# Kernel optimization log

Hardware: AMD Instinct MI355X
Metric: run time of the kernel (lower is better)

The kernel has to match this reference:

```python
import jax, jax.numpy as jnp
import numpy as np

B, Q, N, H, W = 8, 4096, 128, 256, 256
ALPHA = 0.4      # adaptive-bandwidth coefficient
EOS = 0.5        # eos_coef -> empty_weight[0]
DIV_THRS = 0.5   # div threshold for dense stride
EPS = 1e-5


def setup_inputs() -> dict:
    key = jax.random.key(0)
    k = jax.random.split(key, 8)
    pred_logits = jax.random.normal(k[0], (B, Q, 2), jnp.float32)
    pred_points = jax.random.uniform(k[1], (B, Q, 2), jnp.float32)  # normalized [0,1)
    # GT points in pixel coords (col0 scaled by H, col1 by W, matching the code's normalization quirk)
    tgt_points = jax.random.uniform(k[2], (B, N, 2), jnp.float32) * jnp.array([H, W], jnp.float32)
    split_map = jax.random.uniform(k[3], (B, Q), jnp.float32)
    den = jax.random.uniform(k[4], (B,), jnp.float32)
    prob = jax.random.uniform(k[5], (B, 1, H, W), jnp.float32)
    prob_est = jax.random.uniform(k[6], (B, 1, H, W), jnp.float32)
    src_idx = jax.random.randint(k[7], (B, N), 0, Q)  # matched query index per GT point
    labels = jnp.ones((B, N), jnp.int32)  # single foreground class = 1
    return dict(pred_logits=pred_logits, pred_points=pred_points, tgt_points=tgt_points,
                split_map=split_map, den=den, prob=prob, prob_est=prob_est,
                src_idx=src_idx, labels=labels)


def _density_map(tp_norm, batch_idx):
    """Adaptive-bandwidth Gaussian splatting (vectorized KDTree + conv2d replacement).
    tp_norm: (M,2) normalized points; batch_idx: (M,) int. Returns (B,H,W)."""
    M = tp_norm.shape[0]
    # integer pixel locations, as in the original (round + clip before KDTree)
    px = jnp.clip(jnp.round(tp_norm[:, 0] * W), 0, W - 1)
    py = jnp.clip(jnp.round(tp_norm[:, 1] * H), 0, H - 1)
    pts = jnp.stack([px, py], axis=1).reshape(B, N, 2)  # (B,N,2) float pixel coords
    # per-batch pairwise distances -> 4-NN (self included)
    d2 = jnp.sum((pts[:, :, None, :] - pts[:, None, :, :]) ** 2, axis=-1)  # (B,N,N)
    dist = jnp.sqrt(jnp.maximum(d2, 0.0))
    neg_d, nn_idx = jax.lax.top_k(-dist, 4)          # ascending distances
    dists = -neg_d                                    # (B,N,4); [...,0] = self = 0
    di = dists[..., 1]                                # nearest-neighbor distance (B,N)
    nbr = nn_idx[..., 1:]                             # (B,N,3) neighbor indices
    nbr_d = jnp.take_along_axis(jnp.broadcast_to(di[:, None, :], (B, N, N)), nbr, axis=2)
    d_mtop3 = jnp.mean(nbr_d, axis=-1)                # mean of neighbors' NN distances
    d = jnp.minimum(di, d_mtop3)
    sigma = jnp.maximum(ALPHA * d, 1.0).reshape(M)    # (M,)
    # truncation window: kernel_size = int(6*sigma), forced odd; half = ks // 2
    ks = (6.0 * sigma).astype(jnp.int32)
    ks = jnp.where(ks % 2 == 0, ks + 1, ks)
    half = (ks // 2).astype(jnp.float32)              # (M,)
    # peak-normalized truncated Gaussian == exp(-r^2/(2 sigma^2)) inside the kernel window
    yy = jnp.arange(H, dtype=jnp.float32)
    xx = jnp.arange(W, dtype=jnp.float32)
    dyv = yy[None, :] - py[:, None]                   # (M,H)
    dxv = xx[None, :] - px[:, None]                   # (M,W)
    r2 = dyv[:, :, None] ** 2 + dxv[:, None, :] ** 2  # (M,H,W)
    inside = (jnp.abs(dyv) <= half[:, None])[:, :, None] & (jnp.abs(dxv) <= half[:, None])[:, None, :]
    maps = jnp.where(inside, jnp.exp(-r2 / (2.0 * (sigma ** 2)[:, None, None])), 0.0)
    # density = elementwise max over points of a batch (zeros where no point contributes)
    dens = jax.ops.segment_max(maps, batch_idx, num_segments=B, indices_are_sorted=True)
    return jnp.maximum(dens, 0.0)                     # (B,H,W)


def reference(pred_logits, pred_points, tgt_points, split_map, den, prob, prob_est, src_idx, labels):
    f32 = jnp.float32
    batch_idx = jnp.repeat(jnp.arange(B), N)          # (M,)
    src_flat = src_idx.reshape(-1)                    # (M,)

    # ---------------- loss_labels (div variant) ----------------
    target_classes = jnp.zeros((B, Q), jnp.int32).at[batch_idx, src_flat].set(labels.reshape(-1))
    logp = jax.nn.log_softmax(pred_logits, axis=-1)
    raw_ce = -jnp.take_along_axis(logp, target_classes[..., None], axis=-1)[..., 0]  # (B,Q)
    weights = jnp.where(target_classes == 0, EOS, 1.0).astype(f32)
    order = jnp.argsort(den)
    is_sp = jnp.zeros((B,), bool).at[order[B // 2:]].set(True)  # sparse = denser-half images
    sp = is_sp.astype(f32)[:, None]
    ds = 1.0 - sp
    div_m = (split_map > DIV_THRS).astype(f32)
    ndiv_m = (split_map <= DIV_THRS).astype(f32)
    wdm = weights * div_m
    loss_ce = ((raw_ce * wdm * sp).sum() / ((wdm * sp).sum() + EPS)
               + (raw_ce * wdm * ds).sum() / ((wdm * ds).sum() + EPS)
               + (raw_ce * weights * ndiv_m).sum() / ((weights * ndiv_m).sum() + EPS))

    # ---------------- loss_points ('prob' variant, div) ----------------
    src_pts = pred_points[batch_idx, src_flat]        # (M,2)
    tp = tgt_points.reshape(-1, 2) / jnp.array([H, W], f32)  # faithful: col0/img_h, col1/img_w
    density = _density_map(tp, batch_idx)             # (B,H,W)
    # grid_sample(bilinear, align_corners=True) at predicted points
    gx = jnp.clip(src_pts[:, 0] * W, 0.0, W - 1.0)
    gy = jnp.clip(src_pts[:, 1] * H, 0.0, H - 1.0)
    x0 = jnp.floor(gx).astype(jnp.int32); y0 = jnp.floor(gy).astype(jnp.int32)
    x1 = jnp.clip(x0 + 1, 0, W - 1);      y1 = jnp.clip(y0 + 1, 0, H - 1)
    fx = gx - x0; fy = gy - y0
    b = batch_idx
    prob_vals = ((1 - fy) * (1 - fx) * density[b, y0, x0]
                 + (1 - fy) * fx * density[b, y0, x1]
                 + fy * (1 - fx) * density[b, y1, x0]
                 + fy * fx * density[b, y1, x1])      # (M,)
    loss_raw = (1.0 - prob_vals)[:, None] * jnp.ones((1, 2), f32) * 0.05  # (M,2)
    sp_pts = is_sp[batch_idx].astype(f32)
    ds_pts = 1.0 - sp_pts
    div_pts = div_m[batch_idx, src_flat]
    nd_pts = ndiv_m[batch_idx, src_flat]
    ld = loss_raw * div_pts[:, None]
    loss_points = ((ld * sp_pts[:, None]).sum() / (sp_pts.sum() + EPS)
                   + (ld * ds_pts[:, None]).sum() / (ds_pts.sum() + EPS)
                   + (loss_raw * nd_pts[:, None]).sum() / (nd_pts.sum() + EPS))

    # ---------------- loss_maps ----------------
    loss_maps = jnp.mean((prob - prob_est) ** 2)

    return jnp.stack([loss_ce, loss_points, loss_maps])
```

## Files before the change

kernel.cpp:

```cpp
#include <hip/hip_runtime.h>
#include <math.h>

#define B_ 8
#define Q_ 4096
#define N_ 128
#define EPS_ 1e-5f

typedef unsigned int u32;

__device__ __forceinline__ float wave_sum64(float x) {
    #pragma unroll
    for (int o = 32; o > 0; o >>= 1) x += __shfl_xor(x, o, 64);
    return x;
}

__global__ __launch_bounds__(1024) void geom_ce_kernel(
    const float* __restrict__ pred_logits,
    const float* __restrict__ tgt_points,
    const float* __restrict__ split_map,
    const int*   __restrict__ src_idx,
    const int*   __restrict__ labels,
    float4* __restrict__ ws_geom,
    float*  __restrict__ ce_part)
{
    const int b = blockIdx.x;
    const int t = threadIdx.x;
    __shared__ u32   bits[Q_ / 32];
    __shared__ int   spk[N_];
    __shared__ float sdi[N_];
    __shared__ float wred[16 * 4];

    const float4* logitsv = (const float4*)pred_logits;
    const float4* splitv  = (const float4*)split_map;
    float4 L0 = logitsv[b * 2048 + 2 * t];
    float4 L1 = logitsv[b * 2048 + 2 * t + 1];
    float4 S4 = splitv[b * 1024 + t];

    float2 tp = make_float2(0.f, 0.f);
    int src = 0, lab = 0;
    if (t < N_) {
        tp  = ((const float2*)tgt_points)[b * N_ + t];
        src = src_idx[b * N_ + t];
        lab = labels[b * N_ + t];
        bits[t] = 0u;
    }
    __syncthreads();

    if (t < N_) {
        float px = rintf((tp.x / 256.f) * 256.f);
        float py = rintf((tp.y / 256.f) * 256.f);
        px = fminf(fmaxf(px, 0.f), 255.f);
        py = fminf(fmaxf(py, 0.f), 255.f);
        spk[t] = (((int)px) << 8) | ((int)py);
        if (lab != 0) atomicOr(&bits[src >> 5], 1u << (src & 31));
    }
    __syncthreads();

    const int p = t >> 3;
    const int r = t & 7;
    int nb1, nb2, nb3;
    float di;
    {
        int mypk = spk[p];
        int myx = mypk >> 8, myy = mypk & 255;
        u32 s0 = 0x7fffffffu, s1 = 0x7fffffffu, s2 = 0x7fffffffu, s3 = 0x7fffffffu;
        #pragma unroll
        for (int jj = 0; jj < 16; ++jj) {
            int j  = jj * 8 + r;
            int pk = spk[j];
            int dx = (pk >> 8) - myx;
            int dy = (pk & 255) - myy;
            u32 u = ((u32)(dx * dx + dy * dy) << 7) | (u32)j;
            u32 m0 = min(s0, u); u = max(s0, u); s0 = m0;
            u32 m1 = min(s1, u); u = max(s1, u); s1 = m1;
            u32 m2 = min(s2, u); u = max(s2, u); s2 = m2;
            s3 = min(s3, u);
        }
        #pragma unroll
        for (int m = 1; m <= 4; m <<= 1) {
            u32 q0 = (u32)__shfl_xor((int)s0, m, 64);
            u32 q1 = (u32)__shfl_xor((int)s1, m, 64);
            u32 q2 = (u32)__shfl_xor((int)s2, m, 64);
            u32 q3 = (u32)__shfl_xor((int)s3, m, 64);
            u32 l0 = min(s0, q3), l1 = min(s1, q2), l2 = min(s2, q1), l3 = min(s3, q0);
            u32 a0 = min(l0, l2), a2 = max(l0, l2);
            u32 a1 = min(l1, l3), a3 = max(l1, l3);
            s0 = min(a0, a1); s1 = max(a0, a1);
            s2 = min(a2, a3); s3 = max(a2, a3);
        }
        di  = sqrtf((float)(s1 >> 7));
        nb1 = (int)(s1 & 127u); nb2 = (int)(s2 & 127u); nb3 = (int)(s3 & 127u);
        if (r == 0) sdi[p] = di;
    }
    __syncthreads();

    if (r == 0) {
        float dmean = ((sdi[nb1] + sdi[nb2]) + sdi[nb3]) / 3.0f;
        float d     = fminf(di, dmean);
        float sigma = fmaxf(0.4f * d, 1.0f);
        int ks = (int)(6.0f * sigma);
        if ((ks & 1) == 0) ks += 1;
        int pk = spk[p];
        ws_geom[b * N_ + p] = make_float4((float)(pk >> 8), (float)(pk & 255),
                                          (float)(ks / 2), 2.0f * sigma * sigma);
    }

    float lq0[4] = {L0.x, L0.z, L1.x, L1.z};
    float lq1[4] = {L0.y, L0.w, L1.y, L1.w};
    float sm4[4] = {S4.x, S4.y, S4.z, S4.w};
    float s_dn = 0.f, s_dd = 0.f, s_nn = 0.f, s_nd = 0.f;
    #pragma unroll
    for (int k = 0; k < 4; ++k) {
        int q = 4 * t + k;
        float l0 = lq0[k], l1 = lq1[k];
        int   tc = (bits[q >> 5] >> (q & 31)) & 1;
        float mx  = fmaxf(l0, l1);
        float lse = mx + logf(expf(l0 - mx) + expf(l1 - mx));
        float rce = lse - (tc ? l1 : l0);
        float w   = tc ? 1.0f : 0.5f;
        float dmf = (sm4[k] > 0.5f) ? 1.0f : 0.0f;
        s_dn += rce * w * dmf;
        s_dd += w * dmf;
        s_nn += rce * w * (1.0f - dmf);
        s_nd += w * (1.0f - dmf);
    }
    float r0 = wave_sum64(s_dn), r1 = wave_sum64(s_dd);
    float r2 = wave_sum64(s_nn), r3 = wave_sum64(s_nd);
    const int wid = t >> 6;
    if ((t & 63) == 0) {
        wred[wid * 4 + 0] = r0; wred[wid * 4 + 1] = r1;
        wred[wid * 4 + 2] = r2; wred[wid * 4 + 3] = r3;
    }
    __syncthreads();
    if (t == 0) {
        float a0 = 0.f, a1 = 0.f, a2 = 0.f, a3 = 0.f;
        for (int wv = 0; wv < 16; ++wv) {
            a0 += wred[wv * 4 + 0]; a1 += wred[wv * 4 + 1];
            a2 += wred[wv * 4 + 2]; a3 += wred[wv * 4 + 3];
        }
        ce_part[b * 4 + 0] = a0; ce_part[b * 4 + 1] = a1;
        ce_part[b * 4 + 2] = a2; ce_part[b * 4 + 3] = a3;
    }
}

__global__ __launch_bounds__(64) void density_kernel(
    const float* __restrict__ pred_points,
    const float* __restrict__ split_map,
    const int*   __restrict__ src_idx,
    const float4* __restrict__ prob,
    const float4* __restrict__ prob_est,
    const float4* __restrict__ ws_geom,
    float4* __restrict__ ptv4)
{
    const int g = blockIdx.x;
    const int b = g >> 7;
    const int l = threadIdx.x;

    float msum = 0.f;
    {
        int i0 = g * 64 + l;
        float4 x0 = prob[i0],          y0 = prob_est[i0];
        float4 x1 = prob[i0 + 65536],  y1 = prob_est[i0 + 65536];
        float d;
        d = x0.x - y0.x; msum += d * d;  d = x0.y - y0.y; msum += d * d;
        d = x0.z - y0.z; msum += d * d;  d = x0.w - y0.w; msum += d * d;
        d = x1.x - y1.x; msum += d * d;  d = x1.y - y1.y; msum += d * d;
        d = x1.z - y1.z; msum += d * d;  d = x1.w - y1.w; msum += d * d;
    }

    float4 G0 = ws_geom[b * N_ + l];
    float4 G1 = ws_geom[b * N_ + 64 + l];

    int   src = src_idx[g];
    float sx  = pred_points[(b * Q_ + src) * 2 + 0];
    float sy  = pred_points[(b * Q_ + src) * 2 + 1];
    float spl = split_map[b * Q_ + src];
    float gx  = fminf(fmaxf(sx * 256.f, 0.f), 255.f);
    float gy  = fminf(fmaxf(sy * 256.f, 0.f), 255.f);
    int x0 = (int)floorf(gx), y0 = (int)floorf(gy);
    int x1 = min(x0 + 1, 255), y1 = min(y0 + 1, 255);
    float fx = gx - (float)x0, fy = gy - (float)y0;
    float cx0 = (float)x0, cx1 = (float)x1, cy0 = (float)y0, cy1 = (float)y1;

    float c00 = 0.f, c01 = 0.f, c10 = 0.f, c11 = 0.f;
    #pragma unroll
    for (int k = 0; k < 2; ++k) {
        float4 G = k ? G1 : G0;
        float h = G.z, s2 = G.w;
        float dy0 = cy0 - G.y, dy1 = cy1 - G.y;
        float dx0 = cx0 - G.x, dx1 = cx1 - G.x;
        bool iy0 = fabsf(dy0) <= h, iy1 = fabsf(dy1) <= h;
        bool ix0 = fabsf(dx0) <= h, ix1 = fabsf(dx1) <= h;
        if (iy0 && ix0) c00 = fmaxf(c00, expf(-(dy0 * dy0 + dx0 * dx0) / s2));
        if (iy0 && ix1) c01 = fmaxf(c01, expf(-(dy0 * dy0 + dx1 * dx1) / s2));
        if (iy1 && ix0) c10 = fmaxf(c10, expf(-(dy1 * dy1 + dx0 * dx0) / s2));
        if (iy1 && ix1) c11 = fmaxf(c11, expf(-(dy1 * dy1 + dx1 * dx1) / s2));
    }
    #pragma unroll
    for (int o = 32; o > 0; o >>= 1) {
        c00 = fmaxf(c00, __shfl_xor(c00, o, 64));
        c01 = fmaxf(c01, __shfl_xor(c01, o, 64));
        c10 = fmaxf(c10, __shfl_xor(c10, o, 64));
        c11 = fmaxf(c11, __shfl_xor(c11, o, 64));
    }
    msum = wave_sum64(msum);

    if (l == 0) {
        float pv = (1.f - fy) * (1.f - fx) * c00 + (1.f - fy) * fx * c01
                 + fy * (1.f - fx) * c10 + fy * fx * c11;
        float lr   = 0.05f * (1.0f - pv);
        float divf = (spl > 0.5f) ? 1.0f : 0.0f;
        ptv4[g] = make_float4(2.0f * lr * divf, 2.0f * lr * (1.0f - divf),
                              1.0f - divf, msum);
    }
}

__global__ __launch_bounds__(1024) void final_kernel(
    const float*  __restrict__ den,
    const float4* __restrict__ ptv4,
    const float*  __restrict__ ce_part,
    float* __restrict__ out)
{
    __shared__ float4 red[1024];
    const int t = threadIdx.x;
    red[t] = ptv4[t];
    __syncthreads();
    for (int k = 64; k > 0; k >>= 1) {
        if ((t & 127) < k) {
            float4 a = red[t], c = red[t + k];
            red[t] = make_float4(a.x + c.x, a.y + c.y, a.z + c.z, a.w + c.w);
        }
        __syncthreads();
    }
    if (t == 0) {
        float dn[B_];
        for (int i = 0; i < B_; ++i) dn[i] = den[i];

        float mse = 0.f;
        float num_sp = 0.f, den_sp = 0.f, num_ds = 0.f, den_ds = 0.f;
        float num_nd = 0.f, den_nd = 0.f;
        float p_sp = 0.f, p_ds = 0.f, p_nd = 0.f, cnt_nd = 0.f;
        for (int b = 0; b < B_; ++b) {
            int rank = 0;
            for (int j = 0; j < B_; ++j)
                rank += ((dn[j] < dn[b]) || (dn[j] == dn[b] && j < b)) ? 1 : 0;
            float sp  = (rank >= B_ / 2) ? 1.0f : 0.0f;
            float dsv = 1.0f - sp;
            float4 s = red[b * N_];
            mse += s.w;
            float c0 = ce_part[b * 4 + 0], c1 = ce_part[b * 4 + 1];
            float c2 = ce_part[b * 4 + 2], c3 = ce_part[b * 4 + 3];
            num_sp += sp  * c0;  den_sp += sp  * c1;
            num_ds += dsv * c0;  den_ds += dsv * c1;
            num_nd += c2;        den_nd += c3;
            p_sp   += sp  * s.x; p_ds   += dsv * s.x;
            p_nd   += s.y;       cnt_nd += s.z;
        }
        float loss_ce = num_sp / (den_sp + EPS_)
                      + num_ds / (den_ds + EPS_)
                      + num_nd / (den_nd + EPS_);
        float half_cnt = (float)(N_ * (B_ / 2));
        float loss_points = p_sp / (half_cnt + EPS_)
                          + p_ds / (half_cnt + EPS_)
                          + p_nd / (cnt_nd + EPS_);
        out[0] = loss_ce;
        out[1] = loss_points;
        out[2] = mse / (float)(B_ * 256 * 256);
    }
}

extern "C" void kernel_launch(void* const* d_in, const int* in_sizes, int n_in,
                              void* d_out, int out_size, void* d_ws, size_t ws_size,
                              hipStream_t stream) {
    const float* pred_logits = (const float*)d_in[0];
    const float* pred_points = (const float*)d_in[1];
    const float* tgt_points  = (const float*)d_in[2];
    const float* split_map   = (const float*)d_in[3];
    const float* den         = (const float*)d_in[4];
    const float* prob        = (const float*)d_in[5];
    const float* prob_est    = (const float*)d_in[6];
    const int*   src_idx     = (const int*)d_in[7];
    const int*   labels      = (const int*)d_in[8];
    float* out = (float*)d_out;

    char* wsb = (char*)d_ws;
    float4* ws_geom = (float4*)wsb;
    float4* ptv4    = (float4*)(wsb + 16384);
    float*  ce_part = (float*)(wsb + 32768);

    geom_ce_kernel<<<B_, 1024, 0, stream>>>(pred_logits, tgt_points, split_map,
                                            src_idx, labels, ws_geom, ce_part);
    density_kernel<<<B_ * N_, 64, 0, stream>>>(pred_points, split_map, src_idx,
                                               (const float4*)prob,
                                               (const float4*)prob_est,
                                               ws_geom, ptv4);
    final_kernel<<<1, 1024, 0, stream>>>(den, ptv4, ce_part, out);
}
```

Baseline: 17.37 us.

## Fuse geometry, CE, density and MSE into one 256-block kernel with redundant KNN

```diff
diff --git a/kernel.cpp b/kernel.cpp
--- a/kernel.cpp
+++ b/kernel.cpp
@@ -14,34 +14,49 @@
     return x;
 }
 
-__global__ __launch_bounds__(1024) void geom_ce_kernel(
+__global__ __launch_bounds__(1024) void main_kernel(
     const float* __restrict__ pred_logits,
+    const float* __restrict__ pred_points,
     const float* __restrict__ tgt_points,
     const float* __restrict__ split_map,
     const int*   __restrict__ src_idx,
     const int*   __restrict__ labels,
-    float4* __restrict__ ws_geom,
-    float*  __restrict__ ce_part)
+    const float4* __restrict__ prob,
+    const float4* __restrict__ prob_est,
+    float4* __restrict__ part)
 {
-    const int b = blockIdx.x;
+    const int g = blockIdx.x;
+    const int b = g >> 5;
+    const int s = g & 31;
     const int t = threadIdx.x;
-    __shared__ u32   bits[Q_ / 32];
-    __shared__ int   spk[N_];
-    __shared__ float sdi[N_];
-    __shared__ float wred[16 * 4];
-
-    const float4* logitsv = (const float4*)pred_logits;
-    const float4* splitv  = (const float4*)split_map;
-    float4 L0 = logitsv[b * 2048 + 2 * t];
-    float4 L1 = logitsv[b * 2048 + 2 * t + 1];
-    float4 S4 = splitv[b * 1024 + t];
-
+
+    __shared__ u32    bits[Q_ / 32];
+    __shared__ int    spk[N_];
+    __shared__ float  sdi[N_];
+    __shared__ float4 sgeo[N_];
+    __shared__ float  dcor[16];
+    __shared__ float  ptvs[4][3];
+    __shared__ float  wred[16 * 5];
+
+    float4 mseA, mseB;
+    if (t < 512) {
+        int i = g * 512 + t;
+        mseA = prob[i];
+        mseB = prob_est[i];
+    }
+    float l0 = 0.f, l1 = 0.f, smq = 0.f;
+    if (t < 128) {
+        int q = s * 128 + t;
+        l0  = pred_logits[(b * Q_ + q) * 2 + 0];
+        l1  = pred_logits[(b * Q_ + q) * 2 + 1];
+        smq = split_map[b * Q_ + q];
+    }
     float2 tp = make_float2(0.f, 0.f);
-    int src = 0, lab = 0;
+    int srcp = 0, lab = 0;
     if (t < N_) {
-        tp  = ((const float2*)tgt_points)[b * N_ + t];
-        src = src_idx[b * N_ + t];
-        lab = labels[b * N_ + t];
+        tp   = ((const float2*)tgt_points)[b * N_ + t];
+        srcp = src_idx[b * N_ + t];
+        lab  = labels[b * N_ + t];
         bits[t] = 0u;
     }
     __syncthreads();
@@ -52,15 +67,13 @@
         px = fminf(fmaxf(px, 0.f), 255.f);
         py = fminf(fmaxf(py, 0.f), 255.f);
         spk[t] = (((int)px) << 8) | ((int)py);
-        if (lab != 0) atomicOr(&bits[src >> 5], 1u << (src & 31));
-    }
-    __syncthreads();
-
-    const int p = t >> 3;
-    const int r = t & 7;
-    int nb1, nb2, nb3;
-    float di;
+        if (lab != 0) atomicOr(&bits[srcp >> 5], 1u << (srcp & 31));
+    }
+    __syncthreads();
+
     {
+        const int p = t >> 3;
+        const int r = t & 7;
         int mypk = spk[p];
         int myx = mypk >> 8, myy = mypk & 255;
         u32 s0 = 0x7fffffffu, s1 = 0x7fffffffu, s2 = 0x7fffffffu, s3 = 0x7fffffffu;
@@ -82,156 +95,156 @@
             u32 q1 = (u32)__shfl_xor((int)s1, m, 64);
             u32 q2 = (u32)__shfl_xor((int)s2, m, 64);
             u32 q3 = (u32)__shfl_xor((int)s3, m, 64);
-            u32 l0 = min(s0, q3), l1 = min(s1, q2), l2 = min(s2, q1), l3 = min(s3, q0);
-            u32 a0 = min(l0, l2), a2 = max(l0, l2);
-            u32 a1 = min(l1, l3), a3 = max(l1, l3);
+            u32 l0_ = min(s0, q3), l1_ = min(s1, q2), l2_ = min(s2, q1), l3_ = min(s3, q0);
+            u32 a0 = min(l0_, l2_), a2 = max(l0_, l2_);
+            u32 a1 = min(l1_, l3_), a3 = max(l1_, l3_);
             s0 = min(a0, a1); s1 = max(a0, a1);
             s2 = min(a2, a3); s3 = max(a2, a3);
         }
-        di  = sqrtf((float)(s1 >> 7));
-        nb1 = (int)(s1 & 127u); nb2 = (int)(s2 & 127u); nb3 = (int)(s3 & 127u);
+        float di = sqrtf((float)(s1 >> 7));
         if (r == 0) sdi[p] = di;
-    }
-    __syncthreads();
-
-    if (r == 0) {
-        float dmean = ((sdi[nb1] + sdi[nb2]) + sdi[nb3]) / 3.0f;
-        float d     = fminf(di, dmean);
-        float sigma = fmaxf(0.4f * d, 1.0f);
-        int ks = (int)(6.0f * sigma);
-        if ((ks & 1) == 0) ks += 1;
-        int pk = spk[p];
-        ws_geom[b * N_ + p] = make_float4((float)(pk >> 8), (float)(pk & 255),
-                                          (float)(ks / 2), 2.0f * sigma * sigma);
-    }
-
-    float lq0[4] = {L0.x, L0.z, L1.x, L1.z};
-    float lq1[4] = {L0.y, L0.w, L1.y, L1.w};
-    float sm4[4] = {S4.x, S4.y, S4.z, S4.w};
+        __syncthreads();
+        if (r == 0) {
+            int nb1 = (int)(s1 & 127u), nb2 = (int)(s2 & 127u), nb3 = (int)(s3 & 127u);
+            float dmean = ((sdi[nb1] + sdi[nb2]) + sdi[nb3]) / 3.0f;
+            float d     = fminf(di, dmean);
+            float sigma = fmaxf(0.4f * d, 1.0f);
+            int ks = (int)(6.0f * sigma);
+            if ((ks & 1) == 0) ks += 1;
+            sgeo[p] = make_float4((float)(mypk >> 8), (float)(mypk & 255),
+                                  (float)(ks / 2), 2.0f * sigma * sigma);
+        }
+    }
+    __syncthreads();
+
+    {
+        const int w     = t >> 6;
+        const int lw    = t & 63;
+        const int p_loc = w >> 2;
+        const int c     = w & 3;
+        const int n     = s * 4 + p_loc;
+        int   srcn = src_idx[b * N_ + n];
+        float sx = pred_points[(b * Q_ + srcn) * 2 + 0];
+        float sy = pred_points[(b * Q_ + srcn) * 2 + 1];
+        float gx = fminf(fmaxf(sx * 256.f, 0.f), 255.f);
+        float gy = fminf(fmaxf(sy * 256.f, 0.f), 255.f);
+        int x0 = (int)floorf(gx), y0 = (int)floorf(gy);
+        int x1 = min(x0 + 1, 255), y1 = min(y0 + 1, 255);
+        float cx = (float)((c & 1) ? x1 : x0);
+        float cy = (float)((c & 2) ? y1 : y0);
+        float lmax = 0.f;
+        #pragma unroll
+        for (int k = 0; k < 2; ++k) {
+            float4 G = sgeo[lw + 64 * k];
+            float dy = cy - G.y, dx = cx - G.x;
+            if (fabsf(dy) <= G.z && fabsf(dx) <= G.z)
+                lmax = fmaxf(lmax, expf(-(dy * dy + dx * dx) / G.w));
+        }
+        #pragma unroll
+        for (int o = 32; o > 0; o >>= 1)
+            lmax = fmaxf(lmax, __shfl_xor(lmax, o, 64));
+        if (lw == 0) dcor[p_loc * 4 + c] = lmax;
+    }
+    __syncthreads();
+
+    if (t < 4) {
+        const int n = s * 4 + t;
+        int   srcn = src_idx[b * N_ + n];
+        float sx  = pred_points[(b * Q_ + srcn) * 2 + 0];
+        float sy  = pred_points[(b * Q_ + srcn) * 2 + 1];
+        float spl = split_map[b * Q_ + srcn];
+        float gx = fminf(fmaxf(sx * 256.f, 0.f), 255.f);
+        float gy = fminf(fmaxf(sy * 256.f, 0.f), 255.f);
+        int x0 = (int)floorf(gx), y0 = (int)floorf(gy);
+        float fx = gx - (float)x0, fy = gy - (float)y0;
+        float d00 = dcor[t * 4 + 0], d01 = dcor[t * 4 + 1];
+        float d10 = dcor[t * 4 + 2], d11 = dcor[t * 4 + 3];
+        float pv = (1.f - fy) * (1.f - fx) * d00 + (1.f - fy) * fx * d01
+                 + fy * (1.f - fx) * d10 + fy * fx * d11;
+        float lr   = 0.05f * (1.0f - pv);
+        float divf = (spl > 0.5f) ? 1.0f : 0.0f;
+        ptvs[t][0] = 2.0f * lr * divf;
+        ptvs[t][1] = 2.0f * lr * (1.0f - divf);
+        ptvs[t][2] = 1.0f - divf;
+    }
+
     float s_dn = 0.f, s_dd = 0.f, s_nn = 0.f, s_nd = 0.f;
-    #pragma unroll
-    for (int k = 0; k < 4; ++k) {
-        int q = 4 * t + k;
-        float l0 = lq0[k], l1 = lq1[k];
-        int   tc = (bits[q >> 5] >> (q & 31)) & 1;
+    if (t < 128) {
+        int q = s * 128 + t;
+        int tc = (bits[q >> 5] >> (q & 31)) & 1;
         float mx  = fmaxf(l0, l1);
         float lse = mx + logf(expf(l0 - mx) + expf(l1 - mx));
         float rce = lse - (tc ? l1 : l0);
         float w   = tc ? 1.0f : 0.5f;
-        float dmf = (sm4[k] > 0.5f) ? 1.0f : 0.0f;
-        s_dn += rce * w * dmf;
-        s_dd += w * dmf;
-        s_nn += rce * w * (1.0f - dmf);
-        s_nd += w * (1.0f - dmf);
-    }
+        float dmf = (smq > 0.5f) ? 1.0f : 0.0f;
+        s_dn = rce * w * dmf;
+        s_dd = w * dmf;
+        s_nn = rce * w * (1.0f - dmf);
+        s_nd = w * (1.0f - dmf);
+    }
+
+    float msum = 0.f;
+    if (t < 512) {
+        float d;
+        d = mseA.x - mseB.x; msum += d * d;
+        d = mseA.y - mseB.y; msum += d * d;
+        d = mseA.z - mseB.z; msum += d * d;
+        d = mseA.w - mseB.w; msum += d * d;
+    }
+
     float r0 = wave_sum64(s_dn), r1 = wave_sum64(s_dd);
     float r2 = wave_sum64(s_nn), r3 = wave_sum64(s_nd);
+    float r4 = wave_sum64(msum);
     const int wid = t >> 6;
     if ((t & 63) == 0) {
-        wred[wid * 4 + 0] = r0; wred[wid * 4 + 1] = r1;
-        wred[wid * 4 + 2] = r2; wred[wid * 4 + 3] = r3;
+        wred[wid * 5 + 0] = r0; wred[wid * 5 + 1] = r1;
+        wred[wid * 5 + 2] = r2; wred[wid * 5 + 3] = r3;
+        wred[wid * 5 + 4] = r4;
     }
     __syncthreads();
     if (t == 0) {
-        float a0 = 0.f, a1 = 0.f, a2 = 0.f, a3 = 0.f;
+        float a0 = 0.f, a1 = 0.f, a2 = 0.f, a3 = 0.f, a4 = 0.f;
         for (int wv = 0; wv < 16; ++wv) {
-            a0 += wred[wv * 4 + 0]; a1 += wred[wv * 4 + 1];
-            a2 += wred[wv * 4 + 2]; a3 += wred[wv * 4 + 3];
-        }
-        ce_part[b * 4 + 0] = a0; ce_part[b * 4 + 1] = a1;
-        ce_part[b * 4 + 2] = a2; ce_part[b * 4 + 3] = a3;
+            a0 += wred[wv * 5 + 0]; a1 += wred[wv * 5 + 1];
+            a2 += wred[wv * 5 + 2]; a3 += wred[wv * 5 + 3];
+            a4 += wred[wv * 5 + 4];
+        }
+        float p0 = ptvs[0][0] + ptvs[1][0] + ptvs[2][0] + ptvs[3][0];
+        float p1 = ptvs[0][1] + ptvs[1][1] + ptvs[2][1] + ptvs[3][1];
+        float p2 = ptvs[0][2] + ptvs[1][2] + ptvs[2][2] + ptvs[3][2];
+        part[g * 2 + 0] = make_float4(a0, a1, a2, a3);
+        part[g * 2 + 1] = make_float4(p0, p1, p2, a4);
     }
 }
 
-__global__ __launch_bounds__(64) void density_kernel(
-    const float* __restrict__ pred_points,
-    const float* __restrict__ split_map,
-    const int*   __restrict__ src_idx,
-    const float4* __restrict__ prob,
-    const float4* __restrict__ prob_est,
-    const float4* __restrict__ ws_geom,
-    float4* __restrict__ ptv4)
-{
-    const int g = blockIdx.x;
-    const int b = g >> 7;
-    const int l = threadIdx.x;
-
-    float msum = 0.f;
-    {
-        int i0 = g * 64 + l;
-        float4 x0 = prob[i0],          y0 = prob_est[i0];
-        float4 x1 = prob[i0 + 65536],  y1 = prob_est[i0 + 65536];
-        float d;
-        d = x0.x - y0.x; msum += d * d;  d = x0.y - y0.y; msum += d * d;
-        d = x0.z - y0.z; msum += d * d;  d = x0.w - y0.w; msum += d * d;
-        d = x1.x - y1.x; msum += d * d;  d = x1.y - y1.y; msum += d * d;
-        d = x1.z - y1.z; msum += d * d;  d = x1.w - y1.w; msum += d * d;
-    }
-
-    float4 G0 = ws_geom[b * N_ + l];
-    float4 G1 = ws_geom[b * N_ + 64 + l];
-
-    int   src = src_idx[g];
-    float sx  = pred_points[(b * Q_ + src) * 2 + 0];
-    float sy  = pred_points[(b * Q_ + src) * 2 + 1];
-    float spl = split_map[b * Q_ + src];
-    float gx  = fminf(fmaxf(sx * 256.f, 0.f), 255.f);
-    float gy  = fminf(fmaxf(sy * 256.f, 0.f), 255.f);
-    int x0 = (int)floorf(gx), y0 = (int)floorf(gy);
-    int x1 = min(x0 + 1, 255), y1 = min(y0 + 1, 255);
-    float fx = gx - (float)x0, fy = gy - (float)y0;
-    float cx0 = (float)x0, cx1 = (float)x1, cy0 = (float)y0, cy1 = (float)y1;
-
-    float c00 = 0.f, c01 = 0.f, c10 = 0.f, c11 = 0.f;
-    #pragma unroll
-    for (int k = 0; k < 2; ++k) {
-        float4 G = k ? G1 : G0;
-        float h = G.z, s2 = G.w;
-        float dy0 = cy0 - G.y, dy1 = cy1 - G.y;
-        float dx0 = cx0 - G.x, dx1 = cx1 - G.x;
-        bool iy0 = fabsf(dy0) <= h, iy1 = fabsf(dy1) <= h;
-        bool ix0 = fabsf(dx0) <= h, ix1 = fabsf(dx1) <= h;
-        if (iy0 && ix0) c00 = fmaxf(c00, expf(-(dy0 * dy0 + dx0 * dx0) / s2));
-        if (iy0 && ix1) c01 = fmaxf(c01, expf(-(dy0 * dy0 + dx1 * dx1) / s2));
-        if (iy1 && ix0) c10 = fmaxf(c10, expf(-(dy1 * dy1 + dx0 * dx0) / s2));
-        if (iy1 && ix1) c11 = fmaxf(c11, expf(-(dy1 * dy1 + dx1 * dx1) / s2));
-    }
-    #pragma unroll
-    for (int o = 32; o > 0; o >>= 1) {
-        c00 = fmaxf(c00, __shfl_xor(c00, o, 64));
-        c01 = fmaxf(c01, __shfl_xor(c01, o, 64));
-        c10 = fmaxf(c10, __shfl_xor(c10, o, 64));
-        c11 = fmaxf(c11, __shfl_xor(c11, o, 64));
-    }
-    msum = wave_sum64(msum);
-
-    if (l == 0) {
-        float pv = (1.f - fy) * (1.f - fx) * c00 + (1.f - fy) * fx * c01
-                 + fy * (1.f - fx) * c10 + fy * fx * c11;
-        float lr   = 0.05f * (1.0f - pv);
-        float divf = (spl > 0.5f) ? 1.0f : 0.0f;
-        ptv4[g] = make_float4(2.0f * lr * divf, 2.0f * lr * (1.0f - divf),
-                              1.0f - divf, msum);
-    }
-}
-
-__global__ __launch_bounds__(1024) void final_kernel(
+__global__ __launch_bounds__(64) void final_kernel(
     const float*  __restrict__ den,
-    const float4* __restrict__ ptv4,
-    const float*  __restrict__ ce_part,
+    const float4* __restrict__ part,
     float* __restrict__ out)
 {
-    __shared__ float4 red[1024];
     const int t = threadIdx.x;
-    red[t] = ptv4[t];
-    __syncthreads();
-    for (int k = 64; k > 0; k >>= 1) {
-        if ((t & 127) < k) {
-            float4 a = red[t], c = red[t + k];
-            red[t] = make_float4(a.x + c.x, a.y + c.y, a.z + c.z, a.w + c.w);
-        }
-        __syncthreads();
-    }
+    const int bb = t >> 3;
+    const int c  = t & 7;
+    __shared__ float4 bce[B_], bpt[B_];
+
+    float4 A = make_float4(0.f, 0.f, 0.f, 0.f);
+    float4 P = make_float4(0.f, 0.f, 0.f, 0.f);
+    for (int k = 0; k < 4; ++k) {
+        int g = bb * 32 + c * 4 + k;
+        float4 a = part[g * 2 + 0], p = part[g * 2 + 1];
+        A.x += a.x; A.y += a.y; A.z += a.z; A.w += a.w;
+        P.x += p.x; P.y += p.y; P.z += p.z; P.w += p.w;
+    }
+    #pragma unroll
+    for (int o = 1; o <= 4; o <<= 1) {
+        A.x += __shfl_xor(A.x, o, 64); A.y += __shfl_xor(A.y, o, 64);
+        A.z += __shfl_xor(A.z, o, 64); A.w += __shfl_xor(A.w, o, 64);
+        P.x += __shfl_xor(P.x, o, 64); P.y += __shfl_xor(P.y, o, 64);
+        P.z += __shfl_xor(P.z, o, 64); P.w += __shfl_xor(P.w, o, 64);
+    }
+    if (c == 0) { bce[bb] = A; bpt[bb] = P; }
+    __syncthreads();
+
     if (t == 0) {
         float dn[B_];
         for (int i = 0; i < B_; ++i) dn[i] = den[i];
@@ -246,15 +259,13 @@
                 rank += ((dn[j] < dn[b]) || (dn[j] == dn[b] && j < b)) ? 1 : 0;
             float sp  = (rank >= B_ / 2) ? 1.0f : 0.0f;
             float dsv = 1.0f - sp;
-            float4 s = red[b * N_];
-            mse += s.w;
-            float c0 = ce_part[b * 4 + 0], c1 = ce_part[b * 4 + 1];
-            float c2 = ce_part[b * 4 + 2], c3 = ce_part[b * 4 + 3];
-            num_sp += sp  * c0;  den_sp += sp  * c1;
-            num_ds += dsv * c0;  den_ds += dsv * c1;
-            num_nd += c2;        den_nd += c3;
-            p_sp   += sp  * s.x; p_ds   += dsv * s.x;
-            p_nd   += s.y;       cnt_nd += s.z;
+            float4 A2 = bce[b], P2 = bpt[b];
+            mse += P2.w;
+            num_sp += sp  * A2.x;  den_sp += sp  * A2.y;
+            num_ds += dsv * A2.x;  den_ds += dsv * A2.y;
+            num_nd += A2.z;        den_nd += A2.w;
+            p_sp   += sp  * P2.x;  p_ds   += dsv * P2.x;
+            p_nd   += P2.y;        cnt_nd += P2.z;
         }
         float loss_ce = num_sp / (den_sp + EPS_)
                       + num_ds / (den_ds + EPS_)
@@ -283,16 +294,11 @@
     const int*   labels      = (const int*)d_in[8];
     float* out = (float*)d_out;
 
-    char* wsb = (char*)d_ws;
-    float4* ws_geom = (float4*)wsb;
-    float4* ptv4    = (float4*)(wsb + 16384);
-    float*  ce_part = (float*)(wsb + 32768);
-
-    geom_ce_kernel<<<B_, 1024, 0, stream>>>(pred_logits, tgt_points, split_map,
-                                            src_idx, labels, ws_geom, ce_part);
-    density_kernel<<<B_ * N_, 64, 0, stream>>>(pred_points, split_map, src_idx,
-                                               (const float4*)prob,
-                                               (const float4*)prob_est,
-                                               ws_geom, ptv4);
-    final_kernel<<<1, 1024, 0, stream>>>(den, ptv4, ce_part, out);
+    float4* part = (float4*)d_ws;
+
+    main_kernel<<<256, 1024, 0, stream>>>(pred_logits, pred_points, tgt_points,
+                                          split_map, src_idx, labels,
+                                          (const float4*)prob,
+                                          (const float4*)prob_est, part);
+    final_kernel<<<1, 64, 0, stream>>>(den, part, out);
 }
```

After: 14.80 us (median of 2 runs). 14.8% less time.
